# Kernel tuning notes

Hardware: AMD Instinct MI355X
Metric: run time of the kernel (lower is better)

## Reference

```python
import jax, jax.numpy as jnp
import numpy as np
import math

EPS = 1e-5        # matches module-level EPS used to normalize loc
K_PROP = 16       # proposals per element for Wood's rejection sampler (accept rate >>0.5 for m=5)


def _log_ive_1p5(x):
    """log of exponentially-scaled modified Bessel I_{3/2}(x)*exp(-x), closed form for half-integer order.
    I_{3/2}(x) = sqrt(2/(pi x)) * (cosh(x) - sinh(x)/x);  with the exp(-x) scaling
    cosh(x)e^{-x} = (1+e^{-2x})/2 and sinh(x)e^{-x} = (1-e^{-2x})/2."""
    em2 = jnp.exp(-2.0 * x)
    val = jnp.sqrt(2.0 / (jnp.pi * x)) * ((1.0 + em2) * 0.5 - (1.0 - em2) / (2.0 * x))
    return jnp.log(val)


def _vmf_forward(kappa_mu, n_samples, key):
    B, V, m = kappa_mu.shape            # m = vmf_dim + 1 (must be 5 for the closed-form Bessel)
    scale = jnp.linalg.norm(kappa_mu, axis=2, keepdims=True)     # [B,V,1] = kappa
    loc = kappa_mu / (scale + EPS)                               # [B,V,m] unit mean direction

    # --- Wood's rejection sampling constants (as in hyperspherical_vae VonMisesFisher) ---
    c = jnp.sqrt(4.0 * scale ** 2 + (m - 1) ** 2)
    b_true = (-2.0 * scale + c) / (m - 1)
    b_app = (m - 1) / (4.0 * scale)
    s = jnp.clip(scale - 10.0, 0.0, 1.0)          # smooth switch to Taylor approx for large kappa
    b = b_app * s + b_true * (1.0 - s)
    a = (m - 1 + 2.0 * scale + c) / 4.0
    d = (4.0 * a * b) / (1.0 + b) - (m - 1) * math.log(m - 1)

    kb, ku, kv = jax.random.split(key, 3)
    con = (m - 1) / 2.0
    prop_shape = (n_samples, B, V, 1, K_PROP)
    e = jax.random.beta(kb, con, con, prop_shape)                          # Beta proposals
    u = jax.random.uniform(ku, prop_shape, minval=1e-20, maxval=1.0 - 1e-20)
    bb = b[None, ..., None]
    aa = a[None, ..., None]
    dd = d[None, ..., None]
    denom = 1.0 - (1.0 - bb) * e
    w_prop = (1.0 - (1.0 + bb) * e) / denom
    t = (2.0 * aa * bb) / denom
    accept = ((m - 1.0) * jnp.log(t) - t + dd) > jnp.log(u)               # [n,B,V,1,K]
    idx = jnp.argmax(accept, axis=-1)                                      # first accepted proposal
    w = jnp.take_along_axis(w_prop, idx[..., None], axis=-1)[..., 0]       # [n,B,V,1]

    # --- tangent direction + concatenate to sphere point ---
    v = jax.random.normal(kv, (n_samples, B, V, m - 1))
    v = v / jnp.linalg.norm(v, axis=-1, keepdims=True)
    w_ = jnp.sqrt(jnp.clip(1.0 - w ** 2, 1e-10))
    x = jnp.concatenate([w, w_ * v], axis=-1)                              # [n,B,V,m]

    # --- Householder rotation mapping e1 -> loc ---
    e1 = jnp.zeros((m,), dtype=kappa_mu.dtype).at[0].set(1.0)
    uvec = e1 - loc
    uvec = uvec / (jnp.linalg.norm(uvec, axis=-1, keepdims=True) + 1e-5)
    z = x - 2.0 * jnp.sum(x * uvec, axis=-1, keepdims=True) * uvec         # [n,B,V,m]

    # --- log prob under each vMF, summed over the product factors ---
    sc = scale[..., 0]                                                     # [B,V]
    log_unnorm = jnp.sum(loc * z, axis=-1) * sc                            # [n,B,V]
    log_norm = -((m / 2 - 1) * jnp.log(sc) - (m / 2) * math.log(2 * math.pi)
                 - (sc + _log_ive_1p5(sc)))                                 # [B,V]
    log_prob = jnp.sum(log_unnorm - log_norm, axis=-1)                     # [n,B]

    samples = z.reshape(n_samples, B, V * m)                               # [n,B,z_dim]
    return samples.transpose(1, 0, 2), log_prob.transpose(1, 0)            # [B,n,z_dim], [B,n]


def setup_inputs() -> dict:
    key = jax.random.key(0)
    B, V, m = 2048, 64, 5
    kappa_mu = jax.random.normal(key, (B, V, m), dtype=jnp.float32)
    return {"kappa_mu": kappa_mu, "n_samples": 16}


def reference(kappa_mu, n_samples):
    key = jax.random.key(1)
    samples, log_prob = _vmf_forward(kappa_mu, n_samples, key)
    return samples, log_prob
```

## Files before the change

### kernel.cpp

```cpp
#include <hip/hip_runtime.h>
#include <stdint.h>
#include <math.h>

#pragma clang fp contract(off)

struct U2 { uint32_t x, y; };

__host__ __device__ constexpr U2 tf(uint32_t k0, uint32_t k1, uint32_t x0, uint32_t x1) {
  uint32_t k2 = k0 ^ k1 ^ 0x1BD11BDAu;
#define TF_R(r) { x0 += x1; x1 = (x1 << (r)) | (x1 >> (32 - (r))); x1 ^= x0; }
  x0 += k0; x1 += k1;
  TF_R(13) TF_R(15) TF_R(26) TF_R(6)
  x0 += k1; x1 += k2 + 1u;
  TF_R(17) TF_R(29) TF_R(16) TF_R(24)
  x0 += k2; x1 += k0 + 2u;
  TF_R(13) TF_R(15) TF_R(26) TF_R(6)
  x0 += k0; x1 += k1 + 3u;
  TF_R(17) TF_R(29) TF_R(16) TF_R(24)
  x0 += k1; x1 += k2 + 4u;
  TF_R(13) TF_R(15) TF_R(26) TF_R(6)
  x0 += k2; x1 += k0 + 5u;
#undef TF_R
  return U2{x0, x1};
}

__device__ constexpr U2 T0 = tf(0u, 1u, 0u, 0u);
__device__ constexpr U2 T1 = tf(0u, 1u, 0u, 1u);
__device__ constexpr U2 T2 = tf(0u, 1u, 0u, 2u);
__device__ constexpr U2 KA = tf(T0.x, T0.y, 0u, 0u);
__device__ constexpr U2 KB = tf(T0.x, T0.y, 0u, 1u);

__device__ __forceinline__ U2 srow(U2 k, uint32_t i) { return tf(k.x, k.y, 0u, i); }
__device__ __forceinline__ uint32_t rb(U2 k, uint32_t i) {
  U2 r = tf(k.x, k.y, 0u, i); return r.x ^ r.y;
}

__device__ __forceinline__ float u01f(uint32_t b) {
  return __uint_as_float((b >> 9) | 0x3F800000u) - 1.0f;
}

__device__ float log_x(float a) {
  if (a == 0.0f) return -__builtin_inff();
  if (a < 0.0f) return __builtin_nanf("");
  if (__builtin_isinf(a)) return a;
  uint32_t bits = __float_as_uint(a);
  int e = (int)(bits >> 23) - 126;
  float m = __uint_as_float((bits & 0x007FFFFFu) | 0x3F000000u);
  if (m < 0.70710678118654752440f) { e -= 1; m = m + m - 1.0f; }
  else                             { m = m - 1.0f; }
  float z = m * m;
  float y = fmaf(7.0376836292E-2f, m, -1.1514610310E-1f);
  y = fmaf(y, m,  1.1676998740E-1f);
  y = fmaf(y, m, -1.2420140846E-1f);
  y = fmaf(y, m,  1.4249322787E-1f);
  y = fmaf(y, m, -1.6668057665E-1f);
  y = fmaf(y, m,  2.0000714765E-1f);
  y = fmaf(y, m, -2.4999993993E-1f);
  y = fmaf(y, m,  3.3333331174E-1f);
  y = y * m; y = y * z;
  y = fmaf((float)e, -2.12194440e-4f, y);
  y = fmaf(z, -0.5f, y);
  float r = m + y;
  r = fmaf((float)e, 0.693359375f, r);
  return r;
}

__device__ float exp_x(float a) {
  float x = fminf(a, 88.3762626647950f);
  x = fmaxf(x, -88.3762626647949f);
  float fx = floorf(fmaf(x, 1.44269504088896341f, 0.5f));
  x = x - fx * 0.693359375f;
  x = x - fx * (-2.12194440e-4f);
  float z = x * x;
  float y = fmaf(1.9875691500E-4f, x, 1.3981999507E-3f);
  y = fmaf(y, x, 8.3334519073E-3f);
  y = fmaf(y, x, 4.1665795894E-2f);
  y = fmaf(y, x, 1.6666665459E-1f);
  y = fmaf(y, x, 5.0000001201E-1f);
  y = fmaf(y, z, x);
  y = y + 1.0f;
  return ldexpf(y, (int)fx);
}

__device__ __forceinline__ float log1p_x(float x) {
  float u = 1.0f + x;
  if (u == 1.0f) return x;
  return x * (log_x(u) / (u - 1.0f));
}

__device__ float erfinv_x(float x) {
  float w = -log1p_x(-(x * x));
  float p;
  if (w < 5.0f) {
    w = w - 2.5f;
    p = 2.81022636e-08f;
    p = p * w + 3.43273939e-07f;
    p = p * w + (-3.5233877e-06f);
    p = p * w + (-4.39150654e-06f);
    p = p * w + 0.00021858087f;
    p = p * w + (-0.00125372503f);
    p = p * w + (-0.00417768164f);
    p = p * w + 0.246640727f;
    p = p * w + 1.50140941f;
  } else {
    w = sqrtf(w) - 3.0f;
    p = -0.000200214257f;
    p = p * w + 0.000100950558f;
    p = p * w + 0.00134934322f;
    p = p * w + (-0.00367342844f);
    p = p * w + 0.00573950773f;
    p = p * w + (-0.0076224613f);
    p = p * w + 0.00943887047f;
    p = p * w + 1.00167406f;
    p = p * w + 2.83297682f;
  }
  return p * x;
}

#define F_NEG_ALMOST1 (-0.99999994039535522f)
#define F_SQRT2       (1.4142135623730951f)

#define NB   2048
#define NS   16
#define NV   64
#define ZDIM 320
#define SAMPLES_ELEMS (2048ull*16ull*320ull)
#define NSITES (2048u*16u*64u)
#define T_SITES 16u
#define A_THREADS (NSITES / T_SITES)

__global__ __launch_bounds__(256) void sample_w(const float* __restrict__ km,
                                                float* __restrict__ out) {
  const uint32_t gtid = blockIdx.x * 256u + threadIdx.x;

  const float Dg = 2.0f - 0.33333334f;
  const float Cg = 0.33333334f * (1.0f / sqrtf(Dg));
  const float logDg = log_x(Dg);

  uint32_t t = 0;
  bool need_init = true;
  uint32_t site = 0, i = 0;
  int kprop = 0;
  bool phaseB = false;
  U2 k = {0u, 0u};
  float bw = 0.f, aw = 0.f, dw = 0.f, w0 = 0.f, lga = 0.f;

  #pragma unroll 1
  for (int it = 0; it < 60000; ++it) {
    if (__all(t >= T_SITES)) break;
    bool active = (t < T_SITES);
    if (active && need_init) {
      site = gtid * T_SITES + t;
      uint32_t bv = site & (NB * NV - 1u);
      const float* kp = km + (size_t)bv * 5u;
      float m0 = kp[0], m1 = kp[1], m2 = kp[2], m3 = kp[3], m4 = kp[4];
      float kap = sqrtf(m0*m0 + m1*m1 + m2*m2 + m3*m3 + m4*m4);
      float cwv = sqrtf(4.0f * (kap * kap) + 16.0f);
      float b_true = (-2.0f * kap + cwv) / 4.0f;
      float b_app  = 4.0f / (4.0f * kap);
      float ssw = fminf(fmaxf(kap - 10.0f, 0.0f), 1.0f);
      bw = b_app * ssw + b_true * (1.0f - ssw);
      aw = (4.0f + 2.0f * kap + cwv) / 4.0f;
      dw = (4.0f * aw * bw) / (1.0f + bw) - 5.545177444479562f;
      i = site * 16u;
      kprop = 0; phaseB = false;
      k = srow(srow(KA, i), 0u);
      need_init = false;
    }
    if (active) {
      U2 xk = srow(k, 1u);
      U2 Uk = srow(k, 2u);
      U2 sub = srow(xk, 1u);
      float f = u01f(rb(sub, 0u));
      float un = fmaxf(F_NEG_ALMOST1, f * 2.0f + F_NEG_ALMOST1);
      float x = F_SQRT2 * erfinv_x(un);
      float v = 1.0f + x * Cg;
      if (v <= 0.0f) {
        U2 chain = srow(xk, 0u);
        #pragma unroll 1
        for (int r = 0; r < 16 && v <= 0.0f; ++r) {
          U2 sk = srow(chain, 1u);
          chain = srow(chain, 0u);
          float f2 = u01f(rb(sk, 0u));
          float un2 = fmaxf(F_NEG_ALMOST1, f2 * 2.0f + F_NEG_ALMOST1);
          x = F_SQRT2 * erfinv_x(un2);
          v = 1.0f + x * Cg;
        }
      }
      float X = x * x;
      float V = (v * v) * v;
      float lV = log_x(V);
      float U = u01f(rb(Uk, 0u));
      bool c1 = U >= (1.0f - 0.0331f * (X * X));
      bool c2 = log_x(U) >= (X * 0.5f + Dg * ((1.0f - V) + lV));
      if (c1 && c2) {
        k = srow(k, 0u);
      } else {
        float lg = logDg + lV;
        bool finish = false;
        float wres = 0.0f;
        if (!phaseB) {
          lga = lg;
          phaseB = true;
          k = srow(srow(KB, i), 0u);
        } else {
          float lgb = lg;
          float lm = fmaxf(lga, lgb);
          float ea = exp_x(lga - lm);
          float eb = exp_x(lgb - lm);
          float e = ea / (ea + eb);
          float fu = u01f(rb(T1, i));
          float uu = fmaxf(1e-20f, fu * 1.0f + 1e-20f);
          float denom = 1.0f - (1.0f - bw) * e;
          float wp = (1.0f - (1.0f + bw) * e) / denom;
          float tt = (2.0f * aw * bw) / denom;
          float st = 4.0f * log_x(tt) - tt + dw;
          bool acc = st > log_x(uu);
          if (kprop == 0) w0 = wp;
          if (acc) { wres = wp; finish = true; }
          else {
            ++kprop;
            if (kprop == 16) { wres = w0; finish = true; }
            else { ++i; phaseB = false; k = srow(srow(KA, i), 0u); }
          }
        }
        if (finish) {
          uint32_t vv = site & (NV - 1u);
          uint32_t sb = site >> 6;
          uint32_t s  = sb >> 11;
          uint32_t b  = sb & (NB - 1u);
          out[(size_t)(b * NS + s) * ZDIM + (size_t)vv * 5u] = wres;
          ++t;
          need_init = true;
        }
      }
    }
  }
}

__global__ __launch_bounds__(256) void vmf_finish(const float* __restrict__ km,
                                                  float* __restrict__ out) {
  const int tid  = threadIdx.x;
  const int wd   = tid >> 6;
  const int lane = tid & 63;
  const int bs   = blockIdx.x * 4 + wd;
  const int b    = bs >> 4;
  const int s    = bs & 15;
  const int vv   = lane;

  const float* kp = km + ((size_t)b * NV + vv) * 5;
  float m0 = kp[0], m1 = kp[1], m2 = kp[2], m3 = kp[3], m4 = kp[4];
  float kap = sqrtf(m0*m0 + m1*m1 + m2*m2 + m3*m3 + m4*m4);
  float l0 = m0 / (kap + 1e-5f);
  float l1 = m1 / (kap + 1e-5f);
  float l2 = m2 / (kap + 1e-5f);
  float l3 = m3 / (kap + 1e-5f);
  float l4 = m4 / (kap + 1e-5f);

  float* zo = out + (size_t)(b * NS + s) * ZDIM + (size_t)vv * 5;
  float w = zo[0];

  const uint32_t site = ((uint32_t)(s * NB + b) * NV + (uint32_t)vv);
  uint32_t j0 = site * 4u;
  float f, un, n0, n1, n2, n3;
  f = u01f(rb(T2, j0 + 0u)); un = fmaxf(F_NEG_ALMOST1, f*2.0f + F_NEG_ALMOST1); n0 = F_SQRT2*erfinv_x(un);
  f = u01f(rb(T2, j0 + 1u)); un = fmaxf(F_NEG_ALMOST1, f*2.0f + F_NEG_ALMOST1); n1 = F_SQRT2*erfinv_x(un);
  f = u01f(rb(T2, j0 + 2u)); un = fmaxf(F_NEG_ALMOST1, f*2.0f + F_NEG_ALMOST1); n2 = F_SQRT2*erfinv_x(un);
  f = u01f(rb(T2, j0 + 3u)); un = fmaxf(F_NEG_ALMOST1, f*2.0f + F_NEG_ALMOST1); n3 = F_SQRT2*erfinv_x(un);
  float nn = sqrtf(n0*n0 + n1*n1 + n2*n2 + n3*n3);
  n0 /= nn; n1 /= nn; n2 /= nn; n3 /= nn;

  float w_ = sqrtf(fmaxf(1.0f - w * w, 1e-10f));
  float x0 = w, x1 = w_ * n0, x2 = w_ * n1, x3 = w_ * n2, x4 = w_ * n3;

  float u0 = 1.0f - l0, u1 = -l1, u2 = -l2, u3 = -l3, u4 = -l4;
  float un_ = sqrtf(u0*u0 + u1*u1 + u2*u2 + u3*u3 + u4*u4);
  u0 /= (un_ + 1e-5f); u1 /= (un_ + 1e-5f); u2 /= (un_ + 1e-5f);
  u3 /= (un_ + 1e-5f); u4 /= (un_ + 1e-5f);
  float dot = x0*u0 + x1*u1 + x2*u2 + x3*u3 + x4*u4;
  float z0 = x0 - (2.0f * dot) * u0;
  float z1 = x1 - (2.0f * dot) * u1;
  float z2 = x2 - (2.0f * dot) * u2;
  float z3 = x3 - (2.0f * dot) * u3;
  float z4 = x4 - (2.0f * dot) * u4;

  zo[0] = z0; zo[1] = z1; zo[2] = z2; zo[3] = z3; zo[4] = z4;

  float dlz = l0*z0 + l1*z1 + l2*z2 + l3*z3 + l4*z4;
  float lu = dlz * kap;
  float em2 = exp_x(-2.0f * kap);
  float val = sqrtf(2.0f / (3.14159274f * kap)) *
              ((1.0f + em2) * 0.5f - (1.0f - em2) / (2.0f * kap));
  float li = log_x(val);
  float term = lu + ((1.5f * log_x(kap) - 4.594692666023363f) - (kap + li));

  float acc = term;
  #pragma unroll
  for (int off = 1; off < 64; off <<= 1) acc += __shfl_xor(acc, off, 64);
  if (lane == 0) out[SAMPLES_ELEMS + (size_t)(b * NS + s)] = acc;
}

extern "C" void kernel_launch(void* const* d_in, const int* in_sizes, int n_in,
                              void* d_out, int out_size, void* d_ws, size_t ws_size,
                              hipStream_t stream) {
  const float* km = (const float*)d_in[0];
  float* out = (float*)d_out;
  hipLaunchKernelGGL(sample_w,   dim3(A_THREADS / 256), dim3(256), 0, stream, km, out);
  hipLaunchKernelGGL(vmf_finish, dim3(32768 / 4),       dim3(256), 0, stream, km, out);
}
```

Measured before the change: 246.5 us.

## Use wave-level dynamic work queue for rejection sampling sites

Replaces the fixed per-thread assignment of 16 sites with a per-wave pool of 256 sites. Lanes that finish a site claim the next one through a ballot and popcount prefix. The aim is to cut divergence idle time, where a wave waits on its slowest lane's rejection chain, by keeping every lane busy until the pool is drained. It adds ballot overhead on each iteration, and the site-to-lane mapping becomes irregular, which loosens memory coalescing for the km loads and the output stores.

```diff
diff --git a/kernel.cpp b/kernel.cpp
--- a/kernel.cpp
+++ b/kernel.cpp
@@ -126,19 +126,25 @@
 #define ZDIM 320
 #define SAMPLES_ELEMS (2048ull*16ull*320ull)
 #define NSITES (2048u*16u*64u)
-#define T_SITES 16u
-#define A_THREADS (NSITES / T_SITES)
+#define CHUNK  256u
+#define N_WAVES (NSITES / CHUNK)
 
 __global__ __launch_bounds__(256) void sample_w(const float* __restrict__ km,
                                                 float* __restrict__ out) {
-  const uint32_t gtid = blockIdx.x * 256u + threadIdx.x;
+  const int lane = threadIdx.x & 63;
+  const uint32_t wave_id = blockIdx.x * 4u + (threadIdx.x >> 6);
+  const uint32_t base = wave_id * CHUNK;
 
   const float Dg = 2.0f - 0.33333334f;
   const float Cg = 0.33333334f * (1.0f / sqrtf(Dg));
   const float logDg = log_x(Dg);
-
-  uint32_t t = 0;
-  bool need_init = true;
+  const unsigned long long lmask_lt = (1ull << lane) - 1ull;
+
+  uint32_t next = 0;
+  bool need_site = true;
+  bool lane_done = false;
+  bool have = false;
+
   uint32_t site = 0, i = 0;
   int kprop = 0;
   bool phaseB = false;
@@ -146,28 +152,39 @@
   float bw = 0.f, aw = 0.f, dw = 0.f, w0 = 0.f, lga = 0.f;
 
   #pragma unroll 1
-  for (int it = 0; it < 60000; ++it) {
-    if (__all(t >= T_SITES)) break;
-    bool active = (t < T_SITES);
-    if (active && need_init) {
-      site = gtid * T_SITES + t;
-      uint32_t bv = site & (NB * NV - 1u);
-      const float* kp = km + (size_t)bv * 5u;
-      float m0 = kp[0], m1 = kp[1], m2 = kp[2], m3 = kp[3], m4 = kp[4];
-      float kap = sqrtf(m0*m0 + m1*m1 + m2*m2 + m3*m3 + m4*m4);
-      float cwv = sqrtf(4.0f * (kap * kap) + 16.0f);
-      float b_true = (-2.0f * kap + cwv) / 4.0f;
-      float b_app  = 4.0f / (4.0f * kap);
-      float ssw = fminf(fmaxf(kap - 10.0f, 0.0f), 1.0f);
-      bw = b_app * ssw + b_true * (1.0f - ssw);
-      aw = (4.0f + 2.0f * kap + cwv) / 4.0f;
-      dw = (4.0f * aw * bw) / (1.0f + bw) - 5.545177444479562f;
-      i = site * 16u;
-      kprop = 0; phaseB = false;
-      k = srow(srow(KA, i), 0u);
-      need_init = false;
+  for (int it = 0; it < 20000; ++it) {
+    unsigned long long need = __ballot(need_site);
+    if (need) {
+      if (need_site) {
+        uint32_t idx = next + (uint32_t)__popcll(need & lmask_lt);
+        if (idx < CHUNK) {
+          site = base + idx;
+          uint32_t bv = site & (NB * NV - 1u);
+          const float* kp = km + (size_t)bv * 5u;
+          float m0 = kp[0], m1 = kp[1], m2 = kp[2], m3 = kp[3], m4 = kp[4];
+          float kap = sqrtf(m0*m0 + m1*m1 + m2*m2 + m3*m3 + m4*m4);
+          float cwv = sqrtf(4.0f * (kap * kap) + 16.0f);
+          float b_true = (-2.0f * kap + cwv) / 4.0f;
+          float b_app  = 4.0f / (4.0f * kap);
+          float ssw = fminf(fmaxf(kap - 10.0f, 0.0f), 1.0f);
+          bw = b_app * ssw + b_true * (1.0f - ssw);
+          aw = (4.0f + 2.0f * kap + cwv) / 4.0f;
+          dw = (4.0f * aw * bw) / (1.0f + bw) - 5.545177444479562f;
+          i = site * 16u;
+          kprop = 0; phaseB = false;
+          k = srow(srow(KA, i), 0u);
+          have = true;
+        } else {
+          lane_done = true;
+          have = false;
+        }
+        need_site = false;
+      }
+      next += (uint32_t)__popcll(need);
     }
-    if (active) {
+    if (__all(lane_done)) break;
+
+    if (have) {
       U2 xk = srow(k, 1u);
       U2 Uk = srow(k, 2u);
       U2 sub = srow(xk, 1u);
@@ -230,8 +247,8 @@
           uint32_t s  = sb >> 11;
           uint32_t b  = sb & (NB - 1u);
           out[(size_t)(b * NS + s) * ZDIM + (size_t)vv * 5u] = wres;
-          ++t;
-          need_init = true;
+          have = false;
+          need_site = true;
         }
       }
     }
@@ -305,6 +322,6 @@
                               hipStream_t stream) {
   const float* km = (const float*)d_in[0];
   float* out = (float*)d_out;
-  hipLaunchKernelGGL(sample_w,   dim3(A_THREADS / 256), dim3(256), 0, stream, km, out);
-  hipLaunchKernelGGL(vmf_finish, dim3(32768 / 4),       dim3(256), 0, stream, km, out);
-}
+  hipLaunchKernelGGL(sample_w,   dim3(N_WAVES / 4), dim3(256), 0, stream, km, out);
+  hipLaunchKernelGGL(vmf_finish, dim3(32768 / 4),   dim3(256), 0, stream, km, out);
+}
```

Result: faster. 209.2 us (-15.1%).
